# Optimization experiments

Measured on AMD Instinct MI355X. Metric: run time of the kernel, lower is better.

The kernel has to match this reference:

```python
import jax, jax.numpy as jnp
import numpy as np

B, N, L = 1, 2048, 256
DX, DY, H = 1536, 768, 12
D = DX // H  # head_dim = 128
EPS_MOD = 1e-6   # modulated_rmsnorm eps
EPS_QK = 1e-5    # per-head RMSNorm eps


def setup_inputs() -> dict:
    key = jax.random.key(0)
    ks = jax.random.split(key, 16)
    def n(k, shape, s=1.0):
        return jax.random.normal(k, shape, dtype=jnp.float32) * s
    # rotary tables: (N, H, D//2), shared across heads
    pos = jnp.arange(N, dtype=jnp.float32)
    inv_freq = 1.0 / (10000.0 ** (jnp.arange(D // 2, dtype=jnp.float32) / (D // 2)))
    ang = pos[:, None] * inv_freq[None, :]                       # (N, D/2)
    rope_cos = jnp.broadcast_to(jnp.cos(ang)[:, None, :], (N, H, D // 2))
    rope_sin = jnp.broadcast_to(jnp.sin(ang)[:, None, :], (N, H, D // 2))
    return {
        "x": n(ks[0], (B, N, DX)),
        "y": n(ks[1], (B, L, DY)),
        "scale_x": n(ks[2], (B, DX), 0.1),
        "scale_y": n(ks[3], (B, DY), 0.1),
        "rope_cos": rope_cos,
        "rope_sin": rope_sin,
        "Wqkv_x": n(ks[4], (DX, 3 * DX), 0.02),
        "bqkv_x": jnp.zeros((3 * DX,), jnp.float32),
        "Wqkv_y": n(ks[5], (DY, 3 * DX), 0.02),
        "bqkv_y": jnp.zeros((3 * DX,), jnp.float32),
        "q_norm_x_w": jnp.ones((D,), jnp.float32),
        "k_norm_x_w": jnp.ones((D,), jnp.float32),
        "q_norm_y_w": jnp.ones((D,), jnp.float32),
        "k_norm_y_w": jnp.ones((D,), jnp.float32),
        "Wproj_x": n(ks[6], (DX, DX), 0.02),
        "bproj_x": jnp.zeros((DX,), jnp.float32),
        "Wproj_y": n(ks[7], (DX, DY), 0.02),
        "bproj_y": jnp.zeros((DY,), jnp.float32),
    }


def _rms(v, eps):
    return v * jax.lax.rsqrt(jnp.mean(v * v, axis=-1, keepdims=True) + eps)


def _rope(q, cos, sin):
    # q: (B, S, H, D); cos/sin: (S, H, D/2); even/odd interleaved rotation
    qe, qo = q[..., 0::2], q[..., 1::2]
    re = qe * cos - qo * sin
    ro = qe * sin + qo * cos
    return jnp.stack([re, ro], axis=-1).reshape(q.shape)


def reference(x, y, scale_x, scale_y, rope_cos, rope_sin,
              Wqkv_x, bqkv_x, Wqkv_y, bqkv_y,
              q_norm_x_w, k_norm_x_w, q_norm_y_w, k_norm_y_w,
              Wproj_x, bproj_x, Wproj_y, bproj_y):
    b, n, dx = x.shape
    _, l, _ = y.shape
    h, d = H, D
    # --- visual stream ---
    xm = _rms(x, EPS_MOD) * (1.0 + scale_x[:, None, :])          # modulated_rmsnorm
    qkv = (xm @ Wqkv_x + bqkv_x).reshape(b, n, 3, h, d)
    q_x, k_x, v_x = qkv[:, :, 0], qkv[:, :, 1], qkv[:, :, 2]
    q_x = _rope(_rms(q_x, EPS_QK) * q_norm_x_w, rope_cos, rope_sin)
    k_x = _rope(_rms(k_x, EPS_QK) * k_norm_x_w, rope_cos, rope_sin)
    # --- text stream ---
    ym = _rms(y, EPS_MOD) * (1.0 + scale_y[:, None, :])
    qkvy = (ym @ Wqkv_y + bqkv_y).reshape(b, l, 3, h, d)
    q_y, k_y, v_y = qkvy[:, :, 0], qkvy[:, :, 1], qkvy[:, :, 2]
    q_y = _rms(q_y, EPS_QK) * q_norm_y_w
    k_y = _rms(k_y, EPS_QK) * k_norm_y_w
    # --- joint attention over concatenated sequence (B, H, N+L, D) ---
    q = jnp.concatenate([q_x, q_y], axis=1).transpose(0, 2, 1, 3)
    k = jnp.concatenate([k_x, k_y], axis=1).transpose(0, 2, 1, 3)
    v = jnp.concatenate([v_x, v_y], axis=1).transpose(0, 2, 1, 3)
    scale = 1.0 / np.sqrt(d).astype(np.float32)
    attn = jax.nn.softmax(jnp.einsum('bhqd,bhkd->bhqk', q, k) * scale, axis=-1)
    out = jnp.einsum('bhqk,bhkd->bhqd', attn, v)
    out = out.transpose(0, 2, 1, 3).reshape(b, n + l, h * d)
    x_out = out[:, :n] @ Wproj_x + bproj_x
    y_out = out[:, n:] @ Wproj_y + bproj_y
    return (x_out, y_out)
```

## Files before the change

### kernel.cpp

```cpp
#include <hip/hip_runtime.h>

typedef unsigned short u16;
typedef __attribute__((ext_vector_type(8))) short short8;
typedef __attribute__((ext_vector_type(4))) short short4v;
typedef __attribute__((ext_vector_type(4))) float floatx4;

__device__ __forceinline__ u16 f2bf(float f) {
  return (u16)((__float_as_uint(f) + 0x8000u) >> 16);
}
__device__ __forceinline__ float bf2f(u16 v) {
  return __uint_as_float(((unsigned)v) << 16);
}
__device__ __forceinline__ unsigned cvt_pk_bf16(float a, float b) {
  unsigned r;
  asm("v_cvt_pk_bf16_f32 %0, %1, %2" : "=v"(r) : "v"(a), "v"(b));
  return r;
}

#define GLD16(g, l) __builtin_amdgcn_global_load_lds( \
    (const __attribute__((address_space(1))) void*)(g), \
    (__attribute__((address_space(3))) void*)(l), 16, 0, 0)

__global__ __launch_bounds__(256) void prep(const float* __restrict__ W0, u16* __restrict__ T0,
                                            const float* __restrict__ W1, u16* __restrict__ T1,
                                            const float* __restrict__ W2, u16* __restrict__ T2,
                                            const float* __restrict__ W3, u16* __restrict__ T3,
                                            const float* __restrict__ x, const float* __restrict__ scale_x,
                                            const float* __restrict__ y, const float* __restrict__ scale_y,
                                            u16* __restrict__ xm, u16* __restrict__ ym) {
  __shared__ float t[32][33];
  const int z = blockIdx.z;
  if (z < 4) {
    const float* in; u16* out; int K, N;
    switch (z) {
      case 0: in = W0; out = T0; K = 1536; N = 4608; break;
      case 1: in = W1; out = T1; K = 768;  N = 4608; break;
      case 2: in = W2; out = T2; K = 1536; N = 1536; break;
      default: in = W3; out = T3; K = 1536; N = 768; break;
    }
    const int n0 = blockIdx.x * 32, k0 = blockIdx.y * 32;
    if (n0 >= N || k0 >= K) return;
    const int tx = threadIdx.x, ty = threadIdx.y;
#pragma unroll
    for (int i = 0; i < 32; i += 8)
      t[ty + i][tx] = in[(size_t)(k0 + ty + i) * N + n0 + tx];
    __syncthreads();
#pragma unroll
    for (int i = 0; i < 32; i += 8)
      out[(size_t)(n0 + ty + i) * K + k0 + tx] = f2bf(t[tx][ty + i]);
  } else {
    const int row = blockIdx.y * 144 + blockIdx.x;
    if (row >= 2304) return;
    const int tid = threadIdx.y * 32 + threadIdx.x;
    const float* xr; const float* sc; u16* dst; int D;
    if (row < 2048) { D = 1536; xr = x + (size_t)row * D; sc = scale_x; dst = xm + (size_t)row * D; }
    else { D = 768; xr = y + (size_t)(row - 2048) * D; sc = scale_y; dst = ym + (size_t)(row - 2048) * D; }
    float ss = 0.f;
    for (int c = tid; c < D; c += 256) { float v = xr[c]; ss += v * v; }
    for (int off = 32; off > 0; off >>= 1) ss += __shfl_down(ss, off);
    __shared__ float red[4];
    if ((tid & 63) == 0) red[tid >> 6] = ss;
    __syncthreads();
    const float tot = red[0] + red[1] + red[2] + red[3];
    const float r = rsqrtf(tot / (float)D + 1e-6f);
    for (int c = tid; c < D; c += 256)
      dst[c] = f2bf(xr[c] * r * (1.0f + sc[c]));
  }
}

template <bool BOUT>
__global__ __launch_bounds__(256) void gemm2(const u16* __restrict__ A0, const u16* __restrict__ BT0,
                                             const float* __restrict__ bias0, void* __restrict__ C0,
                                             int M0, int N0, int K0,
                                             const u16* __restrict__ A1, const u16* __restrict__ BT1,
                                             const float* __restrict__ bias1, void* __restrict__ C1,
                                             int M1, int N1, int K1) {
  const u16 *A, *BT; const float* bias; void* Cout; int M, N, K;
  if (blockIdx.z == 0) { A = A0; BT = BT0; bias = bias0; Cout = C0; M = M0; N = N0; K = K0; }
  else { A = A1; BT = BT1; bias = bias1; Cout = C1; M = M1; N = N1; K = K1; }
  const int bm = blockIdx.y * 128, bn = blockIdx.x * 128;
  if (bm >= M || bn >= N) return;

  __shared__ __align__(16) u16 As[2][128 * 32];
  __shared__ __align__(16) u16 Bs[2][128 * 32];
  const int tid = threadIdx.x;
  const int lane = tid & 63, wave = tid >> 6;
  const int wm = (wave & 1) * 64, wn = (wave >> 1) * 64;
  const int row16 = lane & 15, quad = lane >> 4;

  floatx4 acc[4][4] = {};
  const int r0 = lane >> 2, c4 = (lane & 3) * 8;
  const u16* Ag0 = A + (size_t)(bm + wave * 16 + r0) * K + c4;
  const u16* Ag1 = A + (size_t)(bm + (wave + 4) * 16 + r0) * K + c4;
  const u16* Bg0 = BT + (size_t)(bn + wave * 16 + r0) * K + c4;
  const u16* Bg1 = BT + (size_t)(bn + (wave + 4) * 16 + r0) * K + c4;
  const int d0 = wave * 512, d1 = (wave + 4) * 512;

  GLD16(Ag0, &As[0][d0]);
  GLD16(Ag1, &As[0][d1]);
  GLD16(Bg0, &Bs[0][d0]);
  GLD16(Bg1, &Bs[0][d1]);

  int cur = 0;
  for (int k0 = 0; k0 < K; k0 += 32) {
    if (k0 + 32 < K) {
      GLD16(Ag0 + k0 + 32, &As[cur ^ 1][d0]);
      GLD16(Ag1 + k0 + 32, &As[cur ^ 1][d1]);
      GLD16(Bg0 + k0 + 32, &Bs[cur ^ 1][d0]);
      GLD16(Bg1 + k0 + 32, &Bs[cur ^ 1][d1]);
      asm volatile("s_waitcnt vmcnt(4)" ::: "memory");
    } else {
      asm volatile("s_waitcnt vmcnt(0)" ::: "memory");
    }
    __builtin_amdgcn_s_barrier();
    asm volatile("" ::: "memory");
    short8 af[4], bf[4];
#pragma unroll
    for (int i = 0; i < 4; i++) {
      af[i] = *(const short8*)&As[cur][(wm + i * 16 + row16) * 32 + quad * 8];
      bf[i] = *(const short8*)&Bs[cur][(wn + i * 16 + row16) * 32 + quad * 8];
    }
#pragma unroll
    for (int mi = 0; mi < 4; mi++)
#pragma unroll
      for (int ni = 0; ni < 4; ni++)
        acc[mi][ni] = __builtin_amdgcn_mfma_f32_16x16x32_bf16(af[mi], bf[ni], acc[mi][ni], 0, 0, 0);
    asm volatile("" ::: "memory");
    __builtin_amdgcn_s_barrier();
    cur ^= 1;
  }
#pragma unroll
  for (int mi = 0; mi < 4; mi++) {
#pragma unroll
    for (int ni = 0; ni < 4; ni++) {
      const int col = bn + wn + ni * 16 + row16;
      const float b = bias[col];
      const int row0 = bm + wm + mi * 16 + quad * 4;
#pragma unroll
      for (int r = 0; r < 4; r++) {
        const float v = acc[mi][ni][r] + b;
        if constexpr (BOUT)
          ((u16*)Cout)[(size_t)(row0 + r) * N + col] = f2bf(v);
        else
          ((float*)Cout)[(size_t)(row0 + r) * N + col] = v;
      }
    }
  }
}

__global__ __launch_bounds__(128) void qkv_post(const u16* __restrict__ qkvx,
                                                const u16* __restrict__ qkvy,
                                                const float* __restrict__ qnwx, const float* __restrict__ knwx,
                                                const float* __restrict__ qnwy, const float* __restrict__ knwy,
                                                const float* __restrict__ rcos, const float* __restrict__ rsin,
                                                u16* __restrict__ Q, u16* __restrict__ Kb, u16* __restrict__ V) {
  const int s = blockIdx.x, h = blockIdx.y, d = threadIdx.x;
  const bool isx = s < 2048;
  const u16* base = isx ? (qkvx + (size_t)s * 4608) : (qkvy + (size_t)(s - 2048) * 4608);
  const float q = bf2f(base[h * 128 + d]);
  const float k = bf2f(base[1536 + h * 128 + d]);
  const u16 v = base[3072 + h * 128 + d];
  __shared__ float redq[2], redk[2];
  float sq = q * q, sk = k * k;
  for (int off = 32; off > 0; off >>= 1) { sq += __shfl_down(sq, off); sk += __shfl_down(sk, off); }
  const int lane = threadIdx.x & 63, w = threadIdx.x >> 6;
  if (lane == 0) { redq[w] = sq; redk[w] = sk; }
  __syncthreads();
  const float rq = rsqrtf((redq[0] + redq[1]) * (1.f / 128.f) + 1e-5f);
  const float rk = rsqrtf((redk[0] + redk[1]) * (1.f / 128.f) + 1e-5f);
  float qn = q * rq * (isx ? qnwx[d] : qnwy[d]);
  float kn = k * rk * (isx ? knwx[d] : knwy[d]);
  if (isx) {
    const int i = d >> 1;
    const float c = rcos[((size_t)s * 12 + h) * 64 + i];
    const float sn = rsin[((size_t)s * 12 + h) * 64 + i];
    const float qo = __shfl_xor(qn, 1);
    const float ko = __shfl_xor(kn, 1);
    qn = (d & 1) ? (qo * sn + qn * c) : (qn * c - qo * sn);
    kn = (d & 1) ? (ko * sn + kn * c) : (kn * c - ko * sn);
  }
  qn *= 0.12751737942f;
  const size_t o = ((size_t)h * 2304 + s) * 128 + d;
  Q[o] = f2bf(qn);
  Kb[o] = f2bf(kn);
  V[o] = v;
}

__global__ __launch_bounds__(256) void vtrans(const u16* __restrict__ V, u16* __restrict__ Vt) {
  __shared__ u16 t[32][33];
  const int h = blockIdx.x, st = blockIdx.y * 32, dt = blockIdx.z * 32;
  const u16* Vh = V + (size_t)h * 2304 * 128;
  u16* Vth = Vt + (size_t)h * 128 * 2304;
  const int tx = threadIdx.x, ty = threadIdx.y;
#pragma unroll
  for (int i = 0; i < 32; i += 8)
    t[ty + i][tx] = Vh[(size_t)(st + ty + i) * 128 + dt + tx];
  __syncthreads();
#pragma unroll
  for (int i = 0; i < 32; i += 8)
    Vth[(size_t)(dt + ty + i) * 2304 + st + tx] = t[tx][ty + i];
}

__global__ __launch_bounds__(256, 3) void attn(const u16* __restrict__ Q, const u16* __restrict__ Kb,
                                               const u16* __restrict__ Vt,
                                               u16* __restrict__ Opart,
                                               float* __restrict__ Mp, float* __restrict__ Lp) {
  const int bid = blockIdx.x;
  const int xcd = bid & 7, local = bid >> 3;
  const int combo = xcd * 6 + local / 18;
  const int qt = local % 18;
  const int h = combo % 12, split = combo / 12;
  const int q0 = qt * 128;
  const int tid = threadIdx.x, lane = tid & 63, wave = tid >> 6;
  const int row16 = lane & 15, quad = lane >> 4;
  const u16* Qh = Q + (size_t)h * 2304 * 128;
  const u16* Kh = Kb + (size_t)h * 2304 * 128;
  const u16* Vh = Vt + (size_t)h * 128 * 2304;

  __shared__ __align__(16) u16 Ks[64 * 128];
  __shared__ __align__(16) u16 Vs[128 * 64];
  __shared__ __align__(16) u16 Ps[4][32 * 64];

  short8 qf[2][4];
#pragma unroll
  for (int g = 0; g < 2; g++) {
    const u16* qrow = Qh + (size_t)(q0 + wave * 32 + g * 16 + row16) * 128;
#pragma unroll
    for (int kk = 0; kk < 4; kk++) qf[g][kk] = *(const short8*)(qrow + kk * 32 + quad * 8);
  }
  floatx4 oacc[2][8] = {};
  float m_i[2] = {-1e30f, -1e30f}, l_i[2] = {0.f, 0.f};

  const u16* Kp[4]; const u16* Vp[4];
#pragma unroll
  for (int i = 0; i < 4; i++) {
    const int j = i * 4 + wave;
    const int krow = j * 4 + (lane >> 4);
    const int kcol = ((lane & 15) ^ (krow & 7)) * 8;
    const int vrow = j * 8 + (lane >> 3);
    const int vcol = ((lane & 7) ^ (vrow & 7)) * 8;
    Kp[i] = Kh + (size_t)krow * 128 + kcol;
    Vp[i] = Vh + (size_t)vrow * 2304 + vcol;
  }
  const int sw = row16 & 7;
  const int kbeg = split * 576, kend = kbeg + 576;

  for (int kt = kbeg; kt < kend; kt += 64) {
    __syncthreads();
#pragma unroll
    for (int i = 0; i < 4; i++) {
      GLD16(Kp[i] + (size_t)kt * 128, Ks + (i * 4 + wave) * 512);
      GLD16(Vp[i] + kt, Vs + (i * 4 + wave) * 512);
    }
    __syncthreads();

    floatx4 sacc[2][4] = {};
#pragma unroll
    for (int mk = 0; mk < 4; mk++) {
#pragma unroll
      for (int kk = 0; kk < 4; kk++) {
        const int c = (4 * kk + quad) ^ sw;
        const short8 kfrag = *(const short8*)&Ks[(mk * 16 + row16) * 128 + c * 8];
        sacc[0][mk] = __builtin_amdgcn_mfma_f32_16x16x32_bf16(kfrag, qf[0][kk], sacc[0][mk], 0, 0, 0);
        sacc[1][mk] = __builtin_amdgcn_mfma_f32_16x16x32_bf16(kfrag, qf[1][kk], sacc[1][mk], 0, 0, 0);
      }
    }
#pragma unroll
    for (int g = 0; g < 2; g++) {
      float mx = sacc[g][0][0];
#pragma unroll
      for (int mk = 0; mk < 4; mk++)
#pragma unroll
        for (int r = 0; r < 4; r++) mx = fmaxf(mx, sacc[g][mk][r]);
      mx = fmaxf(mx, __shfl_xor(mx, 16));
      mx = fmaxf(mx, __shfl_xor(mx, 32));
      if (__any(mx > m_i[g] + 8.f)) {
        const float mnew = fmaxf(m_i[g], mx);
        const float alpha = __builtin_amdgcn_exp2f(m_i[g] - mnew);
        m_i[g] = mnew;
        const float a0 = __shfl(alpha, quad * 4 + 0);
        const float a1 = __shfl(alpha, quad * 4 + 1);
        const float a2 = __shfl(alpha, quad * 4 + 2);
        const float a3 = __shfl(alpha, quad * 4 + 3);
#pragma unroll
        for (int nd = 0; nd < 8; nd++) {
          oacc[g][nd][0] *= a0; oacc[g][nd][1] *= a1; oacc[g][nd][2] *= a2; oacc[g][nd][3] *= a3;
        }
        l_i[g] *= alpha;
      }
      float s = 0.f;
#pragma unroll
      for (int mk = 0; mk < 4; mk++)
#pragma unroll
        for (int r = 0; r < 4; r++) {
          const float p = __builtin_amdgcn_exp2f(sacc[g][mk][r] - m_i[g]);
          sacc[g][mk][r] = p;
          s += p;
        }
      s += __shfl_xor(s, 16);
      s += __shfl_xor(s, 32);
      l_i[g] += s;
    }

#pragma unroll
    for (int g = 0; g < 2; g++)
#pragma unroll
      for (int mk = 0; mk < 4; mk++) {
        const int subp = (4 * mk + quad) ^ (sw << 1);
        uint2 pk;
        pk.x = cvt_pk_bf16(sacc[g][mk][0], sacc[g][mk][1]);
        pk.y = cvt_pk_bf16(sacc[g][mk][2], sacc[g][mk][3]);
        *(uint2*)&Ps[wave][(g * 16 + row16) * 64 + subp * 4] = pk;
      }
    const int pc0 = quad ^ sw, pc1 = (4 + quad) ^ sw;
    short8 pf[2][2];
#pragma unroll
    for (int g = 0; g < 2; g++) {
      pf[g][0] = *(const short8*)&Ps[wave][(g * 16 + row16) * 64 + pc0 * 8];
      pf[g][1] = *(const short8*)&Ps[wave][(g * 16 + row16) * 64 + pc1 * 8];
    }
#pragma unroll
    for (int nd = 0; nd < 8; nd++) {
      const short8 vf0 = *(const short8*)&Vs[(nd * 16 + row16) * 64 + pc0 * 8];
      const short8 vf1 = *(const short8*)&Vs[(nd * 16 + row16) * 64 + pc1 * 8];
      oacc[0][nd] = __builtin_amdgcn_mfma_f32_16x16x32_bf16(pf[0][0], vf0, oacc[0][nd], 0, 0, 0);
      oacc[0][nd] = __builtin_amdgcn_mfma_f32_16x16x32_bf16(pf[0][1], vf1, oacc[0][nd], 0, 0, 0);
      oacc[1][nd] = __builtin_amdgcn_mfma_f32_16x16x32_bf16(pf[1][0], vf0, oacc[1][nd], 0, 0, 0);
      oacc[1][nd] = __builtin_amdgcn_mfma_f32_16x16x32_bf16(pf[1][1], vf1, oacc[1][nd], 0, 0, 0);
    }
  }
#pragma unroll
  for (int g = 0; g < 2; g++) {
    const size_t base = (size_t)(split * 12 + h) * 2304 + q0 + wave * 32 + g * 16;
#pragma unroll
    for (int nd = 0; nd < 8; nd++)
#pragma unroll
      for (int r = 0; r < 4; r++)
        Opart[(base + quad * 4 + r) * 128 + nd * 16 + row16] = f2bf(oacc[g][nd][r]);
    if (lane < 16) { Mp[base + lane] = m_i[g]; Lp[base + lane] = l_i[g]; }
  }
}

__global__ __launch_bounds__(256) void attn_combine(const u16* __restrict__ Opart,
                                                    const float* __restrict__ Mp,
                                                    const float* __restrict__ Lp,
                                                    u16* __restrict__ attnout) {
  const int idx = blockIdx.x * 256 + threadIdx.x;
  const int dd = (idx & 31) * 4;
  const int hq = idx >> 5;
  const int h = hq % 12, q = hq / 12;
  size_t b[4]; float ms[4], ls[4];
  float m = -1e30f;
#pragma unroll
  for (int s = 0; s < 4; s++) {
    b[s] = (size_t)(s * 12 + h) * 2304 + q;
    ms[s] = Mp[b[s]]; ls[s] = Lp[b[s]];
    m = fmaxf(m, ms[s]);
  }
  float w[4], denom = 0.f;
#pragma unroll
  for (int s = 0; s < 4; s++) { w[s] = exp2f(ms[s] - m); denom += ls[s] * w[s]; }
  const float inv = 1.0f / denom;
  float ox = 0.f, oy = 0.f, oz = 0.f, ow = 0.f;
#pragma unroll
  for (int s = 0; s < 4; s++) {
    const short4v o = *(const short4v*)&Opart[b[s] * 128 + dd];
    ox += bf2f((u16)o[0]) * w[s]; oy += bf2f((u16)o[1]) * w[s];
    oz += bf2f((u16)o[2]) * w[s]; ow += bf2f((u16)o[3]) * w[s];
  }
  short4v out;
  out[0] = (short)f2bf(ox * inv);
  out[1] = (short)f2bf(oy * inv);
  out[2] = (short)f2bf(oz * inv);
  out[3] = (short)f2bf(ow * inv);
  *(short4v*)&attnout[(size_t)idx * 4] = out;
}

extern "C" void kernel_launch(void* const* d_in, const int* in_sizes, int n_in,
                              void* d_out, int out_size, void* d_ws, size_t ws_size,
                              hipStream_t stream) {
  const float* x        = (const float*)d_in[0];
  const float* y        = (const float*)d_in[1];
  const float* scale_x  = (const float*)d_in[2];
  const float* scale_y  = (const float*)d_in[3];
  const float* rope_cos = (const float*)d_in[4];
  const float* rope_sin = (const float*)d_in[5];
  const float* Wqkv_x   = (const float*)d_in[6];
  const float* bqkv_x   = (const float*)d_in[7];
  const float* Wqkv_y   = (const float*)d_in[8];
  const float* bqkv_y   = (const float*)d_in[9];
  const float* qnwx     = (const float*)d_in[10];
  const float* knwx     = (const float*)d_in[11];
  const float* qnwy     = (const float*)d_in[12];
  const float* knwy     = (const float*)d_in[13];
  const float* Wproj_x  = (const float*)d_in[14];
  const float* bproj_x  = (const float*)d_in[15];
  const float* Wproj_y  = (const float*)d_in[16];
  const float* bproj_y  = (const float*)d_in[17];
  float* out = (float*)d_out;

  char* ws = (char*)d_ws;
  size_t off = 0;
  auto take = [&](size_t bytes) { char* p = ws + off; off += (bytes + 255) & ~(size_t)255; return p; };
  u16* WqkvxT  = (u16*)take((size_t)4608 * 1536 * 2);
  u16* WqkvyT  = (u16*)take((size_t)4608 * 768 * 2);
  u16* WprojxT = (u16*)take((size_t)1536 * 1536 * 2);
  u16* WprojyT = (u16*)take((size_t)768 * 1536 * 2);
  u16* xm      = (u16*)take((size_t)2048 * 1536 * 2);
  u16* ym      = (u16*)take((size_t)256 * 768 * 2);
  u16* qkvx    = (u16*)take((size_t)2048 * 4608 * 2);
  u16* qkvy    = (u16*)take((size_t)256 * 4608 * 2);
  u16* Qb      = (u16*)take((size_t)12 * 2304 * 128 * 2);
  u16* Kb      = (u16*)take((size_t)12 * 2304 * 128 * 2);
  u16* Vb      = (u16*)take((size_t)12 * 2304 * 128 * 2);
  u16* Vt      = (u16*)take((size_t)12 * 128 * 2304 * 2);
  u16* attnout = (u16*)take((size_t)2304 * 1536 * 2);
  u16* Opart   = (u16*)take((size_t)4 * 12 * 2304 * 128 * 2);
  float* Mp    = (float*)take((size_t)4 * 12 * 2304 * 4);
  float* Lp    = (float*)take((size_t)4 * 12 * 2304 * 4);

  prep<<<dim3(144, 48, 5), dim3(32, 8), 0, stream>>>(Wqkv_x, WqkvxT, Wqkv_y, WqkvyT,
                                                     Wproj_x, WprojxT, Wproj_y, WprojyT,
                                                     x, scale_x, y, scale_y, xm, ym);

  gemm2<true><<<dim3(36, 16, 2), 256, 0, stream>>>(xm, WqkvxT, bqkv_x, qkvx, 2048, 4608, 1536,
                                                   ym, WqkvyT, bqkv_y, qkvy, 256, 4608, 768);

  qkv_post<<<dim3(2304, 12), 128, 0, stream>>>(qkvx, qkvy, qnwx, knwx, qnwy, knwy,
                                               rope_cos, rope_sin, Qb, Kb, Vb);
  vtrans<<<dim3(12, 2304 / 32, 128 / 32), dim3(32, 8), 0, stream>>>(Vb, Vt);

  attn<<<dim3(864), 256, 0, stream>>>(Qb, Kb, Vt, Opart, Mp, Lp);
  attn_combine<<<(2304 * 1536 / 4) / 256, 256, 0, stream>>>(Opart, Mp, Lp, attnout);

  gemm2<false><<<dim3(12, 16, 2), 256, 0, stream>>>(attnout, WprojxT, bproj_x, out, 2048, 1536, 1536,
                                                    attnout + (size_t)2048 * 1536, WprojyT, bproj_y,
                                                    out + (size_t)2048 * 1536, 256, 768, 1536);
  (void)in_sizes; (void)n_in; (void)out_size; (void)ws_size;
}
```

Before: 317.7 us.

## Fuse V transpose into vectorized qkv_post and use three attention KV splits

```diff
diff --git a/kernel.cpp b/kernel.cpp
--- a/kernel.cpp
+++ b/kernel.cpp
@@ -148,57 +148,86 @@
   }
 }
 
-__global__ __launch_bounds__(128) void qkv_post(const u16* __restrict__ qkvx,
+__global__ __launch_bounds__(256) void qkv_post(const u16* __restrict__ qkvx,
                                                 const u16* __restrict__ qkvy,
                                                 const float* __restrict__ qnwx, const float* __restrict__ knwx,
                                                 const float* __restrict__ qnwy, const float* __restrict__ knwy,
                                                 const float* __restrict__ rcos, const float* __restrict__ rsin,
-                                                u16* __restrict__ Q, u16* __restrict__ Kb, u16* __restrict__ V) {
-  const int s = blockIdx.x, h = blockIdx.y, d = threadIdx.x;
+                                                u16* __restrict__ Q, u16* __restrict__ Kb, u16* __restrict__ Vt) {
+  const int s0 = blockIdx.x * 32, h = blockIdx.y;
+  const int tid = threadIdx.x, wave = tid >> 6, lane = tid & 63;
+  const int sl = wave * 8 + (lane >> 3);
+  const int s = s0 + sl;
+  const int d0 = (lane & 7) * 16;
   const bool isx = s < 2048;
   const u16* base = isx ? (qkvx + (size_t)s * 4608) : (qkvy + (size_t)(s - 2048) * 4608);
-  const float q = bf2f(base[h * 128 + d]);
-  const float k = bf2f(base[1536 + h * 128 + d]);
-  const u16 v = base[3072 + h * 128 + d];
-  __shared__ float redq[2], redk[2];
-  float sq = q * q, sk = k * k;
-  for (int off = 32; off > 0; off >>= 1) { sq += __shfl_down(sq, off); sk += __shfl_down(sk, off); }
-  const int lane = threadIdx.x & 63, w = threadIdx.x >> 6;
-  if (lane == 0) { redq[w] = sq; redk[w] = sk; }
+
+  const short8 qv0 = *(const short8*)(base + h * 128 + d0);
+  const short8 qv1 = *(const short8*)(base + h * 128 + d0 + 8);
+  const short8 kv0 = *(const short8*)(base + 1536 + h * 128 + d0);
+  const short8 kv1 = *(const short8*)(base + 1536 + h * 128 + d0 + 8);
+  const short8 vv0 = *(const short8*)(base + 3072 + h * 128 + d0);
+  const short8 vv1 = *(const short8*)(base + 3072 + h * 128 + d0 + 8);
+
+  float q[16], k[16];
+#pragma unroll
+  for (int j = 0; j < 8; j++) {
+    q[j] = bf2f((u16)qv0[j]); q[j + 8] = bf2f((u16)qv1[j]);
+    k[j] = bf2f((u16)kv0[j]); k[j + 8] = bf2f((u16)kv1[j]);
+  }
+  float sq = 0.f, sk = 0.f;
+#pragma unroll
+  for (int j = 0; j < 16; j++) { sq += q[j] * q[j]; sk += k[j] * k[j]; }
+#pragma unroll
+  for (int off = 1; off <= 4; off <<= 1) { sq += __shfl_xor(sq, off); sk += __shfl_xor(sk, off); }
+  const float rq = rsqrtf(sq * (1.f / 128.f) + 1e-5f);
+  const float rk = rsqrtf(sk * (1.f / 128.f) + 1e-5f);
+
+  const float* qw = isx ? qnwx : qnwy;
+  const float* kw = isx ? knwx : knwy;
+#pragma unroll
+  for (int j = 0; j < 16; j++) {
+    q[j] = q[j] * rq * qw[d0 + j];
+    k[j] = k[j] * rk * kw[d0 + j];
+  }
+  if (isx) {
+    const float* cb = rcos + ((size_t)s * 12 + h) * 64 + (d0 >> 1);
+    const float* sb = rsin + ((size_t)s * 12 + h) * 64 + (d0 >> 1);
+#pragma unroll
+    for (int p = 0; p < 8; p++) {
+      const float c = cb[p], sn = sb[p];
+      const float qe = q[2 * p], qo = q[2 * p + 1];
+      const float ke = k[2 * p], ko = k[2 * p + 1];
+      q[2 * p] = qe * c - qo * sn; q[2 * p + 1] = qe * sn + qo * c;
+      k[2 * p] = ke * c - ko * sn; k[2 * p + 1] = ke * sn + ko * c;
+    }
+  }
+  u16 qo16[16], ko16[16];
+#pragma unroll
+  for (int j = 0; j < 16; j++) {
+    qo16[j] = f2bf(q[j] * 0.12751737942f);
+    ko16[j] = f2bf(k[j]);
+  }
+  const size_t o = ((size_t)h * 2304 + s) * 128 + d0;
+  *(short8*)(Q + o) = *(const short8*)&qo16[0];
+  *(short8*)(Q + o + 8) = *(const short8*)&qo16[8];
+  *(short8*)(Kb + o) = *(const short8*)&ko16[0];
+  *(short8*)(Kb + o + 8) = *(const short8*)&ko16[8];
+
+  __shared__ u16 vlds[128][33];
+#pragma unroll
+  for (int j = 0; j < 8; j++) {
+    vlds[d0 + j][sl] = (u16)vv0[j];
+    vlds[d0 + 8 + j][sl] = (u16)vv1[j];
+  }
   __syncthreads();
-  const float rq = rsqrtf((redq[0] + redq[1]) * (1.f / 128.f) + 1e-5f);
-  const float rk = rsqrtf((redk[0] + redk[1]) * (1.f / 128.f) + 1e-5f);
-  float qn = q * rq * (isx ? qnwx[d] : qnwy[d]);
-  float kn = k * rk * (isx ? knwx[d] : knwy[d]);
-  if (isx) {
-    const int i = d >> 1;
-    const float c = rcos[((size_t)s * 12 + h) * 64 + i];
-    const float sn = rsin[((size_t)s * 12 + h) * 64 + i];
-    const float qo = __shfl_xor(qn, 1);
-    const float ko = __shfl_xor(kn, 1);
-    qn = (d & 1) ? (qo * sn + qn * c) : (qn * c - qo * sn);
-    kn = (d & 1) ? (ko * sn + kn * c) : (kn * c - ko * sn);
-  }
-  qn *= 0.12751737942f;
-  const size_t o = ((size_t)h * 2304 + s) * 128 + d;
-  Q[o] = f2bf(qn);
-  Kb[o] = f2bf(kn);
-  V[o] = v;
-}
-
-__global__ __launch_bounds__(256) void vtrans(const u16* __restrict__ V, u16* __restrict__ Vt) {
-  __shared__ u16 t[32][33];
-  const int h = blockIdx.x, st = blockIdx.y * 32, dt = blockIdx.z * 32;
-  const u16* Vh = V + (size_t)h * 2304 * 128;
-  u16* Vth = Vt + (size_t)h * 128 * 2304;
-  const int tx = threadIdx.x, ty = threadIdx.y;
-#pragma unroll
-  for (int i = 0; i < 32; i += 8)
-    t[ty + i][tx] = Vh[(size_t)(st + ty + i) * 128 + dt + tx];
-  __syncthreads();
-#pragma unroll
-  for (int i = 0; i < 32; i += 8)
-    Vth[(size_t)(dt + ty + i) * 2304 + st + tx] = t[tx][ty + i];
+  const int row = tid >> 1, sc = (tid & 1) * 16;
+  u16 tmp[16];
+#pragma unroll
+  for (int j = 0; j < 16; j++) tmp[j] = vlds[row][sc + j];
+  u16* vdst = Vt + ((size_t)h * 128 + row) * 2304 + s0 + sc;
+  *(short8*)vdst = *(const short8*)&tmp[0];
+  *(short8*)(vdst + 8) = *(const short8*)&tmp[8];
 }
 
 __global__ __launch_bounds__(256, 3) void attn(const u16* __restrict__ Q, const u16* __restrict__ Kb,
@@ -207,8 +236,9 @@
                                                float* __restrict__ Mp, float* __restrict__ Lp) {
   const int bid = blockIdx.x;
   const int xcd = bid & 7, local = bid >> 3;
-  const int combo = xcd * 6 + local / 18;
-  const int qt = local % 18;
+  const int slot = local / 18, qt = local % 18;
+  const int combo = slot * 8 + xcd;
+  if (combo >= 36) return;
   const int h = combo % 12, split = combo / 12;
   const int q0 = qt * 128;
   const int tid = threadIdx.x, lane = tid & 63, wave = tid >> 6;
@@ -243,7 +273,7 @@
     Vp[i] = Vh + (size_t)vrow * 2304 + vcol;
   }
   const int sw = row16 & 7;
-  const int kbeg = split * 576, kend = kbeg + 576;
+  const int kbeg = split * 768, kend = kbeg + 768;
 
   for (int kt = kbeg; kt < kend; kt += 64) {
     __syncthreads();
@@ -349,21 +379,21 @@
   const int dd = (idx & 31) * 4;
   const int hq = idx >> 5;
   const int h = hq % 12, q = hq / 12;
-  size_t b[4]; float ms[4], ls[4];
+  size_t b[3]; float ms[3], ls[3];
   float m = -1e30f;
 #pragma unroll
-  for (int s = 0; s < 4; s++) {
+  for (int s = 0; s < 3; s++) {
     b[s] = (size_t)(s * 12 + h) * 2304 + q;
     ms[s] = Mp[b[s]]; ls[s] = Lp[b[s]];
     m = fmaxf(m, ms[s]);
   }
-  float w[4], denom = 0.f;
-#pragma unroll
-  for (int s = 0; s < 4; s++) { w[s] = exp2f(ms[s] - m); denom += ls[s] * w[s]; }
+  float w[3], denom = 0.f;
+#pragma unroll
+  for (int s = 0; s < 3; s++) { w[s] = exp2f(ms[s] - m); denom += ls[s] * w[s]; }
   const float inv = 1.0f / denom;
   float ox = 0.f, oy = 0.f, oz = 0.f, ow = 0.f;
 #pragma unroll
-  for (int s = 0; s < 4; s++) {
+  for (int s = 0; s < 3; s++) {
     const short4v o = *(const short4v*)&Opart[b[s] * 128 + dd];
     ox += bf2f((u16)o[0]) * w[s]; oy += bf2f((u16)o[1]) * w[s];
     oz += bf2f((u16)o[2]) * w[s]; ow += bf2f((u16)o[3]) * w[s];
@@ -412,12 +442,11 @@
   u16* qkvy    = (u16*)take((size_t)256 * 4608 * 2);
   u16* Qb      = (u16*)take((size_t)12 * 2304 * 128 * 2);
   u16* Kb      = (u16*)take((size_t)12 * 2304 * 128 * 2);
-  u16* Vb      = (u16*)take((size_t)12 * 2304 * 128 * 2);
   u16* Vt      = (u16*)take((size_t)12 * 128 * 2304 * 2);
   u16* attnout = (u16*)take((size_t)2304 * 1536 * 2);
-  u16* Opart   = (u16*)take((size_t)4 * 12 * 2304 * 128 * 2);
-  float* Mp    = (float*)take((size_t)4 * 12 * 2304 * 4);
-  float* Lp    = (float*)take((size_t)4 * 12 * 2304 * 4);
+  u16* Opart   = (u16*)take((size_t)3 * 12 * 2304 * 128 * 2);
+  float* Mp    = (float*)take((size_t)3 * 12 * 2304 * 4);
+  float* Lp    = (float*)take((size_t)3 * 12 * 2304 * 4);
 
   prep<<<dim3(144, 48, 5), dim3(32, 8), 0, stream>>>(Wqkv_x, WqkvxT, Wqkv_y, WqkvyT,
                                                      Wproj_x, WprojxT, Wproj_y, WprojyT,
@@ -426,11 +455,10 @@
   gemm2<true><<<dim3(36, 16, 2), 256, 0, stream>>>(xm, WqkvxT, bqkv_x, qkvx, 2048, 4608, 1536,
                                                    ym, WqkvyT, bqkv_y, qkvy, 256, 4608, 768);
 
-  qkv_post<<<dim3(2304, 12), 128, 0, stream>>>(qkvx, qkvy, qnwx, knwx, qnwy, knwy,
-                                               rope_cos, rope_sin, Qb, Kb, Vb);
-  vtrans<<<dim3(12, 2304 / 32, 128 / 32), dim3(32, 8), 0, stream>>>(Vb, Vt);
-
-  attn<<<dim3(864), 256, 0, stream>>>(Qb, Kb, Vt, Opart, Mp, Lp);
+  qkv_post<<<dim3(72, 12), 256, 0, stream>>>(qkvx, qkvy, qnwx, knwx, qnwy, knwy,
+                                             rope_cos, rope_sin, Qb, Kb, Vt);
+
+  attn<<<dim3(720), 256, 0, stream>>>(Qb, Kb, Vt, Opart, Mp, Lp);
   attn_combine<<<(2304 * 1536 / 4) / 256, 256, 0, stream>>>(Opart, Mp, Lp, attnout);
 
   gemm2<false><<<dim3(12, 16, 2), 256, 0, stream>>>(attnout, WprojxT, bproj_x, out, 2048, 1536, 1536,
```

Measured after the change: 299.6 us. 1.06x faster.
